# Kernel tuning notes

Measured on AMD Instinct MI355X. Metric: run time of the kernel, lower is better.

The kernel has to match this reference:

```python
import jax, jax.numpy as jnp
import numpy as np

SKIP = 91
PREEMPH = 0.85
N = 33554432  # 2**25 samples


def setup_inputs() -> dict:
    key = jax.random.key(0)
    sig = jax.random.normal(key, (N,), dtype=jnp.float32) * 0.1
    return {"sig": sig}


def _preemph_scan(y, coef):
    # First-order IIR: out[0] = y[0]; out[i] = y[i] + coef * out[i-1]
    # Expressed as an associative scan over pairs (a, b) representing x -> a*x + b.
    a = jnp.full_like(y, coef)

    def combine(e1, e2):
        a1, b1 = e1
        a2, b2 = e2
        return a1 * a2, b2 + a2 * b1

    _, out = jax.lax.associative_scan(combine, (a, y))
    return out


def reference(sig):
    y = _preemph_scan(sig, jnp.float32(PREEMPH))
    # drop first `skip` samples, zero-pad the tail (same length)
    y = jnp.concatenate([y[SKIP:], jnp.zeros((SKIP,), dtype=y.dtype)])
    out = jnp.clip(32768.0 * y, -32768.0, 32767.0).astype(jnp.int16)
    return out
```

## Files before the change

### kernel.cpp

```cpp
#include <hip/hip_runtime.h>


#define BLOCK   256
#define CH      16
#define TILE    (BLOCK * CH)
#define SKIP    91
#define WARM    71
#define COEF    0.85f
#define LOADN   (TILE + 72)
#define PAD4(p) ((p) + 4 * ((p) >> 5))
#define LDS_F   4688

typedef int v4i __attribute__((ext_vector_type(4)));

__global__ __launch_bounds__(BLOCK) void preemph_kernel(
        const float* __restrict__ sig, int* __restrict__ out, int n) {
    __shared__ float lds[LDS_F];
    const int  tid      = threadIdx.x;
    const long tileBase = (long)blockIdx.x * TILE;
    const long tStart   = tileBase + (SKIP - WARM);

    float4* const l4 = reinterpret_cast<float4*>(lds);

    for (int base = 0; base < LOADN; base += BLOCK * 4) {
        int off = base + tid * 4;
        if (off < LOADN) {
            long t = tStart + off;
            float4 v;
            if (t + 3 < (long)n) {
                v = *reinterpret_cast<const float4*>(sig + t);
            } else {
                v.x = (t + 0 < (long)n) ? sig[t + 0] : 0.f;
                v.y = (t + 1 < (long)n) ? sig[t + 1] : 0.f;
                v.z = (t + 2 < (long)n) ? sig[t + 2] : 0.f;
                v.w = (t + 3 < (long)n) ? sig[t + 3] : 0.f;
            }
            l4[PAD4(off) >> 2] = v;
        }
    }
    __syncthreads();

    const int p0 = tid * CH;
    float acc = 0.f;
    int res[CH];
#pragma unroll
    for (int k = 0; k < 22; ++k) {
        float4 v = l4[PAD4(p0 + 4 * k) >> 2];
#pragma unroll
        for (int c = 0; c < 4; ++c) {
            const int e = 4 * k + c;
            float x = (c == 0) ? v.x : (c == 1) ? v.y : (c == 2) ? v.z : v.w;
            if (e < WARM) {
                acc = fmaf(acc, COEF, x);
            } else if (e < WARM + CH) {
                acc = fmaf(acc, COEF, x);
                float s = acc * 32768.f;
                s = fminf(fmaxf(s, -32768.f), 32767.f);
                res[e - WARM] = (int)s;
            }
        }
    }
    const long oBase = tileBase + p0;
    const long oLim  = (long)n - SKIP;
#pragma unroll
    for (int j = 0; j < CH; ++j)
        if (oBase + j >= oLim) res[j] = 0;
    __syncthreads();

#pragma unroll
    for (int k = 0; k < 4; ++k) {
        float4 v;
        v.x = __int_as_float(res[4 * k + 0]);
        v.y = __int_as_float(res[4 * k + 1]);
        v.z = __int_as_float(res[4 * k + 2]);
        v.w = __int_as_float(res[4 * k + 3]);
        l4[PAD4(p0 + 4 * k) >> 2] = v;
    }
    __syncthreads();

    for (int base = 0; base < TILE; base += BLOCK * 4) {
        int off = base + tid * 4;
        long o  = tileBase + off;
        float4 v = l4[PAD4(off) >> 2];
        v4i iv;
        iv.x = __float_as_int(v.x);
        iv.y = __float_as_int(v.y);
        iv.z = __float_as_int(v.z);
        iv.w = __float_as_int(v.w);
        if (o + 3 < (long)n) {
            __builtin_nontemporal_store(iv, reinterpret_cast<v4i*>(out + o));
        } else {
            if (o + 0 < (long)n) out[o + 0] = iv.x;
            if (o + 1 < (long)n) out[o + 1] = iv.y;
            if (o + 2 < (long)n) out[o + 2] = iv.z;
        }
    }
}

extern "C" void kernel_launch(void* const* d_in, const int* in_sizes, int n_in,
                              void* d_out, int out_size, void* d_ws, size_t ws_size,
                              hipStream_t stream) {
    const float* sig = (const float*)d_in[0];
    int* out = (int*)d_out;
    int n = in_sizes[0];
    int grid = (int)(((long)n + TILE - 1) / TILE);
    preemph_kernel<<<grid, BLOCK, 0, stream>>>(sig, out, n);
}
```

Baseline: 231.6 us.

## Load input directly from global per thread instead of staging through LDS

Each thread now reads its own 88-sample window (71 warm-up plus 16 outputs) straight from global memory with float4 loads. Before, the block cooperatively staged the tile into LDS and then read it back. This removes the LDS staging pass and one barrier, and adds an occupancy hint of 8 blocks per CU. The cost is strided, uncoalesced per-thread global reads of about 5.5x the data, which overlap between threads and should mostly hit in cache. Blocks near the end of the array take a scalar fallback path with per-element bounds checks.

```diff
diff --git a/kernel.cpp b/kernel.cpp
--- a/kernel.cpp
+++ b/kernel.cpp
@@ -7,66 +7,66 @@
 #define SKIP    91
 #define WARM    71
 #define COEF    0.85f
-#define LOADN   (TILE + 72)
+#define NREAD   88
 #define PAD4(p) ((p) + 4 * ((p) >> 5))
-#define LDS_F   4688
+#define LDS_F   4608
 
 typedef int v4i __attribute__((ext_vector_type(4)));
 
-__global__ __launch_bounds__(BLOCK) void preemph_kernel(
+__global__ __launch_bounds__(BLOCK, 8) void preemph_kernel(
         const float* __restrict__ sig, int* __restrict__ out, int n) {
     __shared__ float lds[LDS_F];
     const int  tid      = threadIdx.x;
     const long tileBase = (long)blockIdx.x * TILE;
     const long tStart   = tileBase + (SKIP - WARM);
+    const long g0       = tStart + (long)tid * CH;
 
-    float4* const l4 = reinterpret_cast<float4*>(lds);
+    float acc = 0.f;
+    int   res[CH];
 
-    for (int base = 0; base < LOADN; base += BLOCK * 4) {
-        int off = base + tid * 4;
-        if (off < LOADN) {
-            long t = tStart + off;
-            float4 v;
-            if (t + 3 < (long)n) {
-                v = *reinterpret_cast<const float4*>(sig + t);
-            } else {
-                v.x = (t + 0 < (long)n) ? sig[t + 0] : 0.f;
-                v.y = (t + 1 < (long)n) ? sig[t + 1] : 0.f;
-                v.z = (t + 2 < (long)n) ? sig[t + 2] : 0.f;
-                v.w = (t + 3 < (long)n) ? sig[t + 3] : 0.f;
+    const bool safe = (tStart + (long)(BLOCK - 1) * CH + NREAD) <= (long)n;
+
+    if (safe) {
+        const float4* __restrict__ p = reinterpret_cast<const float4*>(sig + g0);
+#pragma unroll
+        for (int k = 0; k < NREAD / 4; ++k) {
+            float4 v = p[k];
+#pragma unroll
+            for (int c = 0; c < 4; ++c) {
+                const int e = 4 * k + c;
+                float x = (c == 0) ? v.x : (c == 1) ? v.y : (c == 2) ? v.z : v.w;
+                if (e < WARM) {
+                    acc = fmaf(acc, COEF, x);
+                } else if (e < WARM + CH) {
+                    acc = fmaf(acc, COEF, x);
+                    float s = acc * 32768.f;
+                    s = fminf(fmaxf(s, -32768.f), 32767.f);
+                    res[e - WARM] = (int)s;
+                }
             }
-            l4[PAD4(off) >> 2] = v;
         }
-    }
-    __syncthreads();
-
-    const int p0 = tid * CH;
-    float acc = 0.f;
-    int res[CH];
+    } else {
 #pragma unroll
-    for (int k = 0; k < 22; ++k) {
-        float4 v = l4[PAD4(p0 + 4 * k) >> 2];
-#pragma unroll
-        for (int c = 0; c < 4; ++c) {
-            const int e = 4 * k + c;
-            float x = (c == 0) ? v.x : (c == 1) ? v.y : (c == 2) ? v.z : v.w;
-            if (e < WARM) {
-                acc = fmaf(acc, COEF, x);
-            } else if (e < WARM + CH) {
-                acc = fmaf(acc, COEF, x);
+        for (int e = 0; e < WARM + CH; ++e) {
+            long g = g0 + e;
+            float x = (g < (long)n) ? sig[g] : 0.f;
+            acc = fmaf(acc, COEF, x);
+            if (e >= WARM) {
                 float s = acc * 32768.f;
                 s = fminf(fmaxf(s, -32768.f), 32767.f);
                 res[e - WARM] = (int)s;
             }
         }
     }
-    const long oBase = tileBase + p0;
+
+    const long oBase = tileBase + (long)tid * CH;
     const long oLim  = (long)n - SKIP;
 #pragma unroll
     for (int j = 0; j < CH; ++j)
         if (oBase + j >= oLim) res[j] = 0;
-    __syncthreads();
 
+    float4* const l4 = reinterpret_cast<float4*>(lds);
+    const int p0 = tid * CH;
 #pragma unroll
     for (int k = 0; k < 4; ++k) {
         float4 v;
@@ -78,9 +78,10 @@
     }
     __syncthreads();
 
-    for (int base = 0; base < TILE; base += BLOCK * 4) {
-        int off = base + tid * 4;
-        long o  = tileBase + off;
+#pragma unroll
+    for (int k = 0; k < 4; ++k) {
+        int  off = k * (BLOCK * 4) + tid * 4;
+        long o   = tileBase + off;
         float4 v = l4[PAD4(off) >> 2];
         v4i iv;
         iv.x = __float_as_int(v.x);
```

Result: slower. 257.1 us (+11.0%).
